# Kernel optimization log

Measured on AMD Instinct MI355X. Metric: run time of the kernel, lower is better.

Reference implementation:

```python
import jax, jax.numpy as jnp
import numpy as np

TOP_K = 2


def setup_inputs() -> dict:
    key = jax.random.key(0)
    k1, k2, k3, k4, k5 = jax.random.split(key, 5)
    H, F, E = 1024, 2048, 8
    B, S = 2, 1024
    return {
        "hidden_states": jax.random.normal(k1, (B, S, H), dtype=jnp.float32),
        "gate_w": jax.random.normal(k2, (E, H), dtype=jnp.float32) * (1.0 / np.sqrt(H)),
        "w1": jax.random.normal(k3, (E, F, H), dtype=jnp.float32) * (1.0 / np.sqrt(H)),
        "w2": jax.random.normal(k4, (E, H, F), dtype=jnp.float32) * (1.0 / np.sqrt(F)),
        "w3": jax.random.normal(k5, (E, F, H), dtype=jnp.float32) * (1.0 / np.sqrt(H)),
    }


def reference(hidden_states, gate_w, w1, w2, w3):
    B, S, H = hidden_states.shape
    E = gate_w.shape[0]
    x = hidden_states.reshape(-1, H)  # [T, H]

    # Router: softmax in float32, top-k, renormalize (exact Mixtral math)
    router_logits = x @ gate_w.T  # [T, E]
    probs = jax.nn.softmax(router_logits.astype(jnp.float32), axis=-1)
    routing_weights, selected = jax.lax.top_k(probs, TOP_K)  # [T, K]
    routing_weights = routing_weights / routing_weights.sum(axis=-1, keepdims=True)
    routing_weights = routing_weights.astype(x.dtype)

    # Per-token combine weight for each expert: [T, E]
    combine = (jax.nn.one_hot(selected, E, dtype=x.dtype) * routing_weights[..., None]).sum(axis=1)

    # Dense grouped expert SwiGLU MLP (zero combine weight for unselected experts
    # makes this strictly equivalent to the gathered/dispatched computation)
    h = jnp.einsum('th,efh->etf', x, w1)   # [E, T, F]
    g = jnp.einsum('th,efh->etf', x, w3)   # [E, T, F]
    mid = jax.nn.silu(h) * g               # SwiGLU
    expert_out = jnp.einsum('etf,ehf->eth', mid, w2)  # [E, T, H]
    out = jnp.einsum('eth,te->th', expert_out, combine)  # weighted combine

    return out.reshape(B, S, H), router_logits
```

## Files before the change

kernel.cpp:

```cpp
#include <hip/hip_runtime.h>
#include <hip/hip_bf16.h>
#include <math.h>

#define H 1024
#define FF 2048
#define E 8
#define T 2048
#define NSLOT (2*T)
#define SLOT_PAD 128

#define WCONV_BLKS 12288
#define XCONV_BLKS 512
#define ROUTER_BLKS T
#define K1_BLKS (WCONV_BLKS + XCONV_BLKS + ROUTER_BLKS)

typedef __attribute__((ext_vector_type(8))) short s16x8;
typedef __attribute__((ext_vector_type(4))) float f32x4;
typedef __attribute__((ext_vector_type(4))) unsigned int u32x4;

static __device__ __forceinline__ unsigned short f2bf(float f) {
    union { float f; unsigned u; } v; v.f = f;
    unsigned r = v.u + 0x7fff + ((v.u >> 16) & 1);
    return (unsigned short)(r >> 16);
}
static __device__ __forceinline__ float bf2f(unsigned short s) {
    union { unsigned u; float f; } v; v.u = ((unsigned)s) << 16;
    return v.f;
}
static __device__ __forceinline__ unsigned pack2(float a, float b) {
    return (unsigned)f2bf(a) | ((unsigned)f2bf(b) << 16);
}

typedef __attribute__((address_space(3))) unsigned int lds_uint;
typedef const __attribute__((address_space(1))) unsigned int glob_uint;
static __device__ __forceinline__ void gl_lds16(const void* g, void* l) {
    __builtin_amdgcn_global_load_lds((glob_uint*)g, (lds_uint*)l, 16, 0, 0);
}

static __device__ __forceinline__ void expert_range(const int* __restrict__ counts,
                                                    int e, int& off, int& cnt) {
    int acc = 0;
    #pragma unroll
    for (int i = 0; i < E; ++i) {
        int c = counts[i];
        if (i < e) acc += c;
        if (i == e) cnt = c;
    }
    off = acc;
}

__global__ __launch_bounds__(256) void prep_kernel(
    const float* __restrict__ x, const float* __restrict__ gw,
    const float* __restrict__ w1, const float* __restrict__ w3,
    const float* __restrict__ w2,
    unsigned short* __restrict__ w1b, unsigned short* __restrict__ w3b,
    unsigned short* __restrict__ w2b, unsigned short* __restrict__ xb,
    float* __restrict__ logits_out, int* __restrict__ top_id,
    float* __restrict__ top_w, int* __restrict__ counts)
{
    int b = blockIdx.x;
    int tid = threadIdx.x;
    if (b < WCONV_BLKS + XCONV_BLKS) {
        const float* s; unsigned short* d; size_t i;
        if (b < WCONV_BLKS) {
            int r = b >> 12;
            s = (r == 0) ? w1 : (r == 1) ? w3 : w2;
            d = (r == 0) ? w1b : (r == 1) ? w3b : w2b;
            i = ((size_t)(b & 4095) * 256 + tid) * 16;
        } else {
            s = x; d = xb;
            i = ((size_t)(b - WCONV_BLKS) * 256 + tid) * 16;
        }
        f32x4 a0 = __builtin_nontemporal_load((const f32x4*)(s + i));
        f32x4 a1 = __builtin_nontemporal_load((const f32x4*)(s + i + 4));
        f32x4 a2 = __builtin_nontemporal_load((const f32x4*)(s + i + 8));
        f32x4 a3 = __builtin_nontemporal_load((const f32x4*)(s + i + 12));
        u32x4 r0, r1;
        r0.x = pack2(a0.x, a0.y); r0.y = pack2(a0.z, a0.w);
        r0.z = pack2(a1.x, a1.y); r0.w = pack2(a1.z, a1.w);
        r1.x = pack2(a2.x, a2.y); r1.y = pack2(a2.z, a2.w);
        r1.z = pack2(a3.x, a3.y); r1.w = pack2(a3.z, a3.w);
        *(u32x4*)(d + i) = r0;
        *(u32x4*)(d + i + 8) = r1;
        return;
    }
    int t = b - (WCONV_BLKS + XCONV_BLKS);
    int e = tid >> 5;
    int l32 = tid & 31;
    const float* xr = x + (size_t)t * H;
    const float* gr = gw + (size_t)e * H;
    float s = 0.f;
    for (int h = l32; h < H; h += 32) s += xr[h] * gr[h];
    for (int off = 16; off; off >>= 1) s += __shfl_down(s, off, 32);
    __shared__ float lg[E];
    if (l32 == 0) lg[e] = s;
    __syncthreads();
    if (tid < E) logits_out[(size_t)t * E + tid] = lg[tid];
    if (tid == 0) {
        int i1 = 0; float b1 = lg[0];
        for (int i = 1; i < E; ++i) if (lg[i] > b1) { b1 = lg[i]; i1 = i; }
        int i2 = -1; float b2 = -INFINITY;
        for (int i = 0; i < E; ++i) if (i != i1 && lg[i] > b2) { b2 = lg[i]; i2 = i; }
        float p2 = expf(b2 - b1);
        float inv = 1.f / (1.f + p2);
        top_id[2*t]   = i1;  top_id[2*t+1] = i2;
        top_w[2*t]    = inv; top_w[2*t+1]  = p2 * inv;
        atomicAdd(&counts[i1], 1);
        atomicAdd(&counts[i2], 1);
    }
}

__global__ __launch_bounds__(256) void assign_kernel(
    const int* __restrict__ top_id, const int* __restrict__ counts,
    int* __restrict__ cursors, int* __restrict__ top_pos,
    int* __restrict__ slot_token)
{
    int t = blockIdx.x * 256 + threadIdx.x;
    if (t >= T) return;
    int offs[E];
    {
        int acc = 0;
        #pragma unroll
        for (int i = 0; i < E; ++i) { offs[i] = acc; acc += counts[i]; }
    }
    #pragma unroll
    for (int k = 0; k < 2; ++k) {
        int e = top_id[2*t + k];
        int p = offs[e] + atomicAdd(&cursors[e], 1);
        top_pos[2*t + k] = p;
        slot_token[p] = t;
    }
}

__global__ __launch_bounds__(256) void gemm1_kernel(
    const unsigned short* __restrict__ xb, const int* __restrict__ slot_token,
    const unsigned short* __restrict__ w1b, const unsigned short* __restrict__ w3b,
    const int* __restrict__ counts, unsigned short* __restrict__ mid)
{
    int e = blockIdx.z;
    int off, cnt;
    expert_range(counts, e, off, cnt);
    int m0 = blockIdx.y * 128;
    if (m0 >= cnt) return;
    int f0 = blockIdx.x * 64;

    __shared__ __align__(16) unsigned short sx[128 * 64];
    __shared__ __align__(16) unsigned short s1[64 * 64];
    __shared__ __align__(16) unsigned short s3[64 * 64];

    int tid = threadIdx.x;
    int wv = tid >> 6, ln = tid & 63;
    int quad = ln >> 4, l16 = ln & 15;
    int wm = wv & 1, wn = wv >> 1;
    int xor7 = l16 & 7;

    const unsigned short* xsrc[4]; unsigned short* xdst[4];
    #pragma unroll
    for (int j = 0; j < 4; ++j) {
        int row = wv * 32 + j * 8 + (ln >> 3);
        int slot = off + m0 + row;
        if (m0 + row >= cnt) slot = off;
        int tok = slot_token[slot];
        int cl = (ln & 7) ^ (row & 7);
        xsrc[j] = xb + (size_t)tok * H + cl * 8;
        xdst[j] = &sx[(wv * 32 + j * 8) * 64];
    }
    const unsigned short *w1s[2], *w3s[2]; unsigned short *d1[2], *d3[2];
    #pragma unroll
    for (int j = 0; j < 2; ++j) {
        int row = wv * 16 + j * 8 + (ln >> 3);
        int cl = (ln & 7) ^ (row & 7);
        w1s[j] = w1b + ((size_t)e * FF + f0 + row) * H + cl * 8;
        w3s[j] = w3b + ((size_t)e * FF + f0 + row) * H + cl * 8;
        d1[j] = &s1[(wv * 16 + j * 8) * 64];
        d3[j] = &s3[(wv * 16 + j * 8) * 64];
    }

    f32x4 acc1[4][2], acc3[4][2];
    #pragma unroll
    for (int i = 0; i < 4; ++i)
        #pragma unroll
        for (int j = 0; j < 2; ++j) {
            acc1[i][j] = (f32x4){0.f, 0.f, 0.f, 0.f};
            acc3[i][j] = (f32x4){0.f, 0.f, 0.f, 0.f};
        }

    for (int k0 = 0; k0 < H; k0 += 64) {
        #pragma unroll
        for (int j = 0; j < 4; ++j) gl_lds16(xsrc[j] + k0, xdst[j]);
        #pragma unroll
        for (int j = 0; j < 2; ++j) { gl_lds16(w1s[j] + k0, d1[j]); gl_lds16(w3s[j] + k0, d3[j]); }
        __syncthreads();
        #pragma unroll
        for (int ks = 0; ks < 2; ++ks) {
            int cph = ((quad + 4 * ks) ^ xor7) << 3;
            s16x8 a[4], b1v[2], b3v[2];
            #pragma unroll
            for (int i = 0; i < 4; ++i)
                a[i] = *(const s16x8*)&sx[(wm * 64 + i * 16 + l16) * 64 + cph];
            #pragma unroll
            for (int j = 0; j < 2; ++j) {
                b1v[j] = *(const s16x8*)&s1[(wn * 32 + j * 16 + l16) * 64 + cph];
                b3v[j] = *(const s16x8*)&s3[(wn * 32 + j * 16 + l16) * 64 + cph];
            }
            #pragma unroll
            for (int i = 0; i < 4; ++i)
                #pragma unroll
                for (int j = 0; j < 2; ++j) {
                    acc1[i][j] = __builtin_amdgcn_mfma_f32_16x16x32_bf16(a[i], b1v[j], acc1[i][j], 0, 0, 0);
                    acc3[i][j] = __builtin_amdgcn_mfma_f32_16x16x32_bf16(a[i], b3v[j], acc3[i][j], 0, 0, 0);
                }
        }
        __syncthreads();
    }

    #pragma unroll
    for (int i = 0; i < 4; ++i) {
        #pragma unroll
        for (int r = 0; r < 4; ++r) {
            int row = wm * 64 + i * 16 + quad * 4 + r;
            if (m0 + row < cnt) {
                size_t base = (size_t)(off + m0 + row) * FF + f0 + wn * 32;
                #pragma unroll
                for (int j = 0; j < 2; ++j) {
                    float h = acc1[i][j][r];
                    float g = acc3[i][j][r];
                    float v = h / (1.f + __expf(-h)) * g;
                    mid[base + j * 16 + l16] = f2bf(v);
                }
            }
        }
    }
}

__global__ __launch_bounds__(256) void gemm2_kernel(
    const unsigned short* __restrict__ mid, const unsigned short* __restrict__ w2b,
    const int* __restrict__ counts, unsigned short* __restrict__ y)
{
    int e = blockIdx.z;
    int off, cnt;
    expert_range(counts, e, off, cnt);
    int m0 = blockIdx.y * 128;
    if (m0 >= cnt) return;
    int n0 = blockIdx.x * 64;

    __shared__ __align__(16) unsigned short sa[128 * 64];
    __shared__ __align__(16) unsigned short sb[64 * 64];

    int tid = threadIdx.x;
    int wv = tid >> 6, ln = tid & 63;
    int quad = ln >> 4, l16 = ln & 15;
    int wm = wv & 1, wn = wv >> 1;
    int xor7 = l16 & 7;

    const unsigned short* asrc[4]; unsigned short* adst[4];
    #pragma unroll
    for (int j = 0; j < 4; ++j) {
        int row = wv * 32 + j * 8 + (ln >> 3);
        int cl = (ln & 7) ^ (row & 7);
        asrc[j] = mid + (size_t)(off + m0 + row) * FF + cl * 8;
        adst[j] = &sa[(wv * 32 + j * 8) * 64];
    }
    const unsigned short* bsrc[2]; unsigned short* bdst[2];
    #pragma unroll
    for (int j = 0; j < 2; ++j) {
        int row = wv * 16 + j * 8 + (ln >> 3);
        int cl = (ln & 7) ^ (row & 7);
        bsrc[j] = w2b + ((size_t)e * H + n0 + row) * FF + cl * 8;
        bdst[j] = &sb[(wv * 16 + j * 8) * 64];
    }

    f32x4 acc[4][2];
    #pragma unroll
    for (int i = 0; i < 4; ++i)
        #pragma unroll
        for (int j = 0; j < 2; ++j) acc[i][j] = (f32x4){0.f, 0.f, 0.f, 0.f};

    for (int k0 = 0; k0 < FF; k0 += 64) {
        #pragma unroll
        for (int j = 0; j < 4; ++j) gl_lds16(asrc[j] + k0, adst[j]);
        #pragma unroll
        for (int j = 0; j < 2; ++j) gl_lds16(bsrc[j] + k0, bdst[j]);
        __syncthreads();
        #pragma unroll
        for (int ks = 0; ks < 2; ++ks) {
            int cph = ((quad + 4 * ks) ^ xor7) << 3;
            s16x8 a[4], b[2];
            #pragma unroll
            for (int i = 0; i < 4; ++i)
                a[i] = *(const s16x8*)&sa[(wm * 64 + i * 16 + l16) * 64 + cph];
            #pragma unroll
            for (int j = 0; j < 2; ++j)
                b[j] = *(const s16x8*)&sb[(wn * 32 + j * 16 + l16) * 64 + cph];
            #pragma unroll
            for (int i = 0; i < 4; ++i)
                #pragma unroll
                for (int j = 0; j < 2; ++j)
                    acc[i][j] = __builtin_amdgcn_mfma_f32_16x16x32_bf16(a[i], b[j], acc[i][j], 0, 0, 0);
        }
        __syncthreads();
    }

    #pragma unroll
    for (int i = 0; i < 4; ++i) {
        #pragma unroll
        for (int r = 0; r < 4; ++r) {
            int row = wm * 64 + i * 16 + quad * 4 + r;
            if (m0 + row < cnt) {
                size_t base = (size_t)(off + m0 + row) * H + n0 + wn * 32;
                #pragma unroll
                for (int j = 0; j < 2; ++j)
                    y[base + j * 16 + l16] = f2bf(acc[i][j][r]);
            }
        }
    }
}

__global__ __launch_bounds__(256) void combine_kernel(
    const unsigned short* __restrict__ y, const int* __restrict__ top_pos,
    const float* __restrict__ top_w, float* __restrict__ out)
{
    int t = blockIdx.x, tid = threadIdx.x;
    int p0 = top_pos[2*t], p1 = top_pos[2*t+1];
    float w0 = top_w[2*t], w1 = top_w[2*t+1];
    ushort4 a = ((const ushort4*)(y + (size_t)p0 * H))[tid];
    ushort4 b = ((const ushort4*)(y + (size_t)p1 * H))[tid];
    float4 o;
    o.x = w0 * bf2f(a.x) + w1 * bf2f(b.x);
    o.y = w0 * bf2f(a.y) + w1 * bf2f(b.y);
    o.z = w0 * bf2f(a.z) + w1 * bf2f(b.z);
    o.w = w0 * bf2f(a.w) + w1 * bf2f(b.w);
    ((float4*)(out + (size_t)t * H))[tid] = o;
}

extern "C" void kernel_launch(void* const* d_in, const int* in_sizes, int n_in,
                              void* d_out, int out_size, void* d_ws, size_t ws_size,
                              hipStream_t stream) {
    const float* x  = (const float*)d_in[0];
    const float* gw = (const float*)d_in[1];
    const float* w1 = (const float*)d_in[2];
    const float* w2 = (const float*)d_in[3];
    const float* w3 = (const float*)d_in[4];
    float* out    = (float*)d_out;
    float* logits = out + (size_t)T * H;

    int* counts      = (int*)d_ws;
    int* cursors     = counts + 8;
    int* top_id      = counts + 16;
    int* top_pos     = top_id + 2*T;
    int* slot_token  = top_pos + 2*T;
    float* top_w     = (float*)(slot_token + NSLOT);
    unsigned short* xb  = (unsigned short*)(top_w + 2*T);
    unsigned short* mid = xb  + (size_t)T * H;
    unsigned short* y   = mid + (size_t)(NSLOT + SLOT_PAD) * FF;
    unsigned short* w1b = y   + (size_t)NSLOT * H;
    unsigned short* w3b = w1b + (size_t)E * FF * H;
    unsigned short* w2b = w3b + (size_t)E * FF * H;

    (void)hipMemsetAsync(counts, 0, 16 * sizeof(int), stream);

    prep_kernel<<<K1_BLKS, 256, 0, stream>>>(x, gw, w1, w3, w2,
                                             w1b, w3b, w2b, xb,
                                             logits, top_id, top_w, counts);
    assign_kernel<<<(T + 255) / 256, 256, 0, stream>>>(top_id, counts, cursors,
                                                       top_pos, slot_token);
    gemm1_kernel<<<dim3(FF / 64, 16, E), 256, 0, stream>>>(xb, slot_token,
                                                           w1b, w3b, counts, mid);
    gemm2_kernel<<<dim3(H / 64, 16, E), 256, 0, stream>>>(mid, w2b, counts, y);
    combine_kernel<<<T, 256, 0, stream>>>(y, top_pos, top_w, out);
}
```

Baseline: 422.2 us.

## Widen expert GEMM N-tiles to 128 and use grid-stride weight conversion

Both grouped GEMM kernels now compute 128x128 output tiles instead of 128x64, so each wave keeps a 4x4 accumulator set and the A tile staged in LDS is reused across twice as many columns. This halves the number of blocks and the redundant loads of token/mid rows. The fp32-to-bf16 prep now uses a fixed 2048-block grid-stride loop over all weight and activation chunks, with plain loads instead of nontemporal ones. Register pressure in gemm1 roughly doubles (32 accumulator vectors), which may lower occupancy, and the smaller grid may underfill the GPU.

Measured after the change: 445.1 us. +5.4%, slower.

```diff
diff --git a/kernel.cpp b/kernel.cpp
--- a/kernel.cpp
+++ b/kernel.cpp
@@ -9,10 +9,11 @@
 #define NSLOT (2*T)
 #define SLOT_PAD 128
 
-#define WCONV_BLKS 12288
-#define XCONV_BLKS 512
-#define ROUTER_BLKS T
-#define K1_BLKS (WCONV_BLKS + XCONV_BLKS + ROUTER_BLKS)
+#define WELEM (E*FF*H)
+#define XELEM (T*H)
+#define TOT_CHUNKS ((3*(size_t)WELEM + XELEM) / 8)
+#define CONV_BLKS 2048
+#define K1_BLKS (CONV_BLKS + T)
 
 typedef __attribute__((ext_vector_type(8))) short s16x8;
 typedef __attribute__((ext_vector_type(4))) float f32x4;
@@ -29,6 +30,12 @@
 }
 static __device__ __forceinline__ unsigned pack2(float a, float b) {
     return (unsigned)f2bf(a) | ((unsigned)f2bf(b) << 16);
+}
+static __device__ __forceinline__ u32x4 pack8(f32x4 a, f32x4 b) {
+    u32x4 r;
+    r.x = pack2(a.x, a.y); r.y = pack2(a.z, a.w);
+    r.z = pack2(b.x, b.y); r.w = pack2(b.z, b.w);
+    return r;
 }
 
 typedef __attribute__((address_space(3))) unsigned int lds_uint;
@@ -60,31 +67,22 @@
 {
     int b = blockIdx.x;
     int tid = threadIdx.x;
-    if (b < WCONV_BLKS + XCONV_BLKS) {
-        const float* s; unsigned short* d; size_t i;
-        if (b < WCONV_BLKS) {
-            int r = b >> 12;
-            s = (r == 0) ? w1 : (r == 1) ? w3 : w2;
-            d = (r == 0) ? w1b : (r == 1) ? w3b : w2b;
-            i = ((size_t)(b & 4095) * 256 + tid) * 16;
-        } else {
-            s = x; d = xb;
-            i = ((size_t)(b - WCONV_BLKS) * 256 + tid) * 16;
-        }
-        f32x4 a0 = __builtin_nontemporal_load((const f32x4*)(s + i));
-        f32x4 a1 = __builtin_nontemporal_load((const f32x4*)(s + i + 4));
-        f32x4 a2 = __builtin_nontemporal_load((const f32x4*)(s + i + 8));
-        f32x4 a3 = __builtin_nontemporal_load((const f32x4*)(s + i + 12));
-        u32x4 r0, r1;
-        r0.x = pack2(a0.x, a0.y); r0.y = pack2(a0.z, a0.w);
-        r0.z = pack2(a1.x, a1.y); r0.w = pack2(a1.z, a1.w);
-        r1.x = pack2(a2.x, a2.y); r1.y = pack2(a2.z, a2.w);
-        r1.z = pack2(a3.x, a3.y); r1.w = pack2(a3.z, a3.w);
-        *(u32x4*)(d + i) = r0;
-        *(u32x4*)(d + i + 8) = r1;
+    if (b < CONV_BLKS) {
+        for (size_t c = (size_t)b * 256 + tid; c < TOT_CHUNKS; c += (size_t)CONV_BLKS * 256) {
+            size_t base = c * 8;
+            int tsel = (int)(base >> 24);
+            const float* s; unsigned short* d; size_t o;
+            if (tsel == 0)      { s = w1; d = w1b; o = base; }
+            else if (tsel == 1) { s = w3; d = w3b; o = base - (size_t)WELEM; }
+            else if (tsel == 2) { s = w2; d = w2b; o = base - 2*(size_t)WELEM; }
+            else                { s = x;  d = xb;  o = base - 3*(size_t)WELEM; }
+            f32x4 a0 = *(const f32x4*)(s + o);
+            f32x4 a1 = *(const f32x4*)(s + o + 4);
+            *(u32x4*)(d + o) = pack8(a0, a1);
+        }
         return;
     }
-    int t = b - (WCONV_BLKS + XCONV_BLKS);
+    int t = b - CONV_BLKS;
     int e = tid >> 5;
     int l32 = tid & 31;
     const float* xr = x + (size_t)t * H;
@@ -142,11 +140,11 @@
     expert_range(counts, e, off, cnt);
     int m0 = blockIdx.y * 128;
     if (m0 >= cnt) return;
-    int f0 = blockIdx.x * 64;
+    int f0 = blockIdx.x * 128;
 
     __shared__ __align__(16) unsigned short sx[128 * 64];
-    __shared__ __align__(16) unsigned short s1[64 * 64];
-    __shared__ __align__(16) unsigned short s3[64 * 64];
+    __shared__ __align__(16) unsigned short s1[128 * 64];
+    __shared__ __align__(16) unsigned short s3[128 * 64];
 
     int tid = threadIdx.x;
     int wv = tid >> 6, ln = tid & 63;
@@ -165,48 +163,50 @@
         xsrc[j] = xb + (size_t)tok * H + cl * 8;
         xdst[j] = &sx[(wv * 32 + j * 8) * 64];
     }
-    const unsigned short *w1s[2], *w3s[2]; unsigned short *d1[2], *d3[2];
-    #pragma unroll
-    for (int j = 0; j < 2; ++j) {
-        int row = wv * 16 + j * 8 + (ln >> 3);
+    const unsigned short *w1s[4], *w3s[4]; unsigned short *d1[4], *d3[4];
+    #pragma unroll
+    for (int j = 0; j < 4; ++j) {
+        int row = wv * 32 + j * 8 + (ln >> 3);
         int cl = (ln & 7) ^ (row & 7);
         w1s[j] = w1b + ((size_t)e * FF + f0 + row) * H + cl * 8;
         w3s[j] = w3b + ((size_t)e * FF + f0 + row) * H + cl * 8;
-        d1[j] = &s1[(wv * 16 + j * 8) * 64];
-        d3[j] = &s3[(wv * 16 + j * 8) * 64];
-    }
-
-    f32x4 acc1[4][2], acc3[4][2];
+        d1[j] = &s1[(wv * 32 + j * 8) * 64];
+        d3[j] = &s3[(wv * 32 + j * 8) * 64];
+    }
+
+    f32x4 acc1[4][4], acc3[4][4];
     #pragma unroll
     for (int i = 0; i < 4; ++i)
         #pragma unroll
-        for (int j = 0; j < 2; ++j) {
+        for (int j = 0; j < 4; ++j) {
             acc1[i][j] = (f32x4){0.f, 0.f, 0.f, 0.f};
             acc3[i][j] = (f32x4){0.f, 0.f, 0.f, 0.f};
         }
 
     for (int k0 = 0; k0 < H; k0 += 64) {
         #pragma unroll
-        for (int j = 0; j < 4; ++j) gl_lds16(xsrc[j] + k0, xdst[j]);
-        #pragma unroll
-        for (int j = 0; j < 2; ++j) { gl_lds16(w1s[j] + k0, d1[j]); gl_lds16(w3s[j] + k0, d3[j]); }
+        for (int j = 0; j < 4; ++j) {
+            gl_lds16(xsrc[j] + k0, xdst[j]);
+            gl_lds16(w1s[j] + k0, d1[j]);
+            gl_lds16(w3s[j] + k0, d3[j]);
+        }
         __syncthreads();
         #pragma unroll
         for (int ks = 0; ks < 2; ++ks) {
             int cph = ((quad + 4 * ks) ^ xor7) << 3;
-            s16x8 a[4], b1v[2], b3v[2];
+            s16x8 a[4], b1v[4], b3v[4];
             #pragma unroll
             for (int i = 0; i < 4; ++i)
                 a[i] = *(const s16x8*)&sx[(wm * 64 + i * 16 + l16) * 64 + cph];
             #pragma unroll
-            for (int j = 0; j < 2; ++j) {
-                b1v[j] = *(const s16x8*)&s1[(wn * 32 + j * 16 + l16) * 64 + cph];
-                b3v[j] = *(const s16x8*)&s3[(wn * 32 + j * 16 + l16) * 64 + cph];
+            for (int j = 0; j < 4; ++j) {
+                b1v[j] = *(const s16x8*)&s1[(wn * 64 + j * 16 + l16) * 64 + cph];
+                b3v[j] = *(const s16x8*)&s3[(wn * 64 + j * 16 + l16) * 64 + cph];
             }
             #pragma unroll
             for (int i = 0; i < 4; ++i)
                 #pragma unroll
-                for (int j = 0; j < 2; ++j) {
+                for (int j = 0; j < 4; ++j) {
                     acc1[i][j] = __builtin_amdgcn_mfma_f32_16x16x32_bf16(a[i], b1v[j], acc1[i][j], 0, 0, 0);
                     acc3[i][j] = __builtin_amdgcn_mfma_f32_16x16x32_bf16(a[i], b3v[j], acc3[i][j], 0, 0, 0);
                 }
@@ -220,9 +220,9 @@
         for (int r = 0; r < 4; ++r) {
             int row = wm * 64 + i * 16 + quad * 4 + r;
             if (m0 + row < cnt) {
-                size_t base = (size_t)(off + m0 + row) * FF + f0 + wn * 32;
+                size_t base = (size_t)(off + m0 + row) * FF + f0 + wn * 64;
                 #pragma unroll
-                for (int j = 0; j < 2; ++j) {
+                for (int j = 0; j < 4; ++j) {
                     float h = acc1[i][j][r];
                     float g = acc3[i][j][r];
                     float v = h / (1.f + __expf(-h)) * g;
@@ -242,10 +242,10 @@
     expert_range(counts, e, off, cnt);
     int m0 = blockIdx.y * 128;
     if (m0 >= cnt) return;
-    int n0 = blockIdx.x * 64;
+    int n0 = blockIdx.x * 128;
 
     __shared__ __align__(16) unsigned short sa[128 * 64];
-    __shared__ __align__(16) unsigned short sb[64 * 64];
+    __shared__ __align__(16) unsigned short sb[128 * 64];
 
     int tid = threadIdx.x;
     int wv = tid >> 6, ln = tid & 63;
@@ -261,41 +261,42 @@
         asrc[j] = mid + (size_t)(off + m0 + row) * FF + cl * 8;
         adst[j] = &sa[(wv * 32 + j * 8) * 64];
     }
-    const unsigned short* bsrc[2]; unsigned short* bdst[2];
-    #pragma unroll
-    for (int j = 0; j < 2; ++j) {
-        int row = wv * 16 + j * 8 + (ln >> 3);
+    const unsigned short* bsrc[4]; unsigned short* bdst[4];
+    #pragma unroll
+    for (int j = 0; j < 4; ++j) {
+        int row = wv * 32 + j * 8 + (ln >> 3);
         int cl = (ln & 7) ^ (row & 7);
         bsrc[j] = w2b + ((size_t)e * H + n0 + row) * FF + cl * 8;
-        bdst[j] = &sb[(wv * 16 + j * 8) * 64];
-    }
-
-    f32x4 acc[4][2];
+        bdst[j] = &sb[(wv * 32 + j * 8) * 64];
+    }
+
+    f32x4 acc[4][4];
     #pragma unroll
     for (int i = 0; i < 4; ++i)
         #pragma unroll
-        for (int j = 0; j < 2; ++j) acc[i][j] = (f32x4){0.f, 0.f, 0.f, 0.f};
+        for (int j = 0; j < 4; ++j) acc[i][j] = (f32x4){0.f, 0.f, 0.f, 0.f};
 
     for (int k0 = 0; k0 < FF; k0 += 64) {
         #pragma unroll
-        for (int j = 0; j < 4; ++j) gl_lds16(asrc[j] + k0, adst[j]);
-        #pragma unroll
-        for (int j = 0; j < 2; ++j) gl_lds16(bsrc[j] + k0, bdst[j]);
+        for (int j = 0; j < 4; ++j) {
+            gl_lds16(asrc[j] + k0, adst[j]);
+            gl_lds16(bsrc[j] + k0, bdst[j]);
+        }
         __syncthreads();
         #pragma unroll
         for (int ks = 0; ks < 2; ++ks) {
             int cph = ((quad + 4 * ks) ^ xor7) << 3;
-            s16x8 a[4], b[2];
+            s16x8 a[4], b[4];
             #pragma unroll
             for (int i = 0; i < 4; ++i)
                 a[i] = *(const s16x8*)&sa[(wm * 64 + i * 16 + l16) * 64 + cph];
             #pragma unroll
-            for (int j = 0; j < 2; ++j)
-                b[j] = *(const s16x8*)&sb[(wn * 32 + j * 16 + l16) * 64 + cph];
+            for (int j = 0; j < 4; ++j)
+                b[j] = *(const s16x8*)&sb[(wn * 64 + j * 16 + l16) * 64 + cph];
             #pragma unroll
             for (int i = 0; i < 4; ++i)
                 #pragma unroll
-                for (int j = 0; j < 2; ++j)
+                for (int j = 0; j < 4; ++j)
                     acc[i][j] = __builtin_amdgcn_mfma_f32_16x16x32_bf16(a[i], b[j], acc[i][j], 0, 0, 0);
         }
         __syncthreads();
@@ -307,9 +308,9 @@
         for (int r = 0; r < 4; ++r) {
             int row = wm * 64 + i * 16 + quad * 4 + r;
             if (m0 + row < cnt) {
-                size_t base = (size_t)(off + m0 + row) * H + n0 + wn * 32;
+                size_t base = (size_t)(off + m0 + row) * H + n0 + wn * 64;
                 #pragma unroll
-                for (int j = 0; j < 2; ++j)
+                for (int j = 0; j < 4; ++j)
                     y[base + j * 16 + l16] = f2bf(acc[i][j][r]);
             }
         }
@@ -354,8 +355,8 @@
     unsigned short* mid = xb  + (size_t)T * H;
     unsigned short* y   = mid + (size_t)(NSLOT + SLOT_PAD) * FF;
     unsigned short* w1b = y   + (size_t)NSLOT * H;
-    unsigned short* w3b = w1b + (size_t)E * FF * H;
-    unsigned short* w2b = w3b + (size_t)E * FF * H;
+    unsigned short* w3b = w1b + (size_t)WELEM;
+    unsigned short* w2b = w3b + (size_t)WELEM;
 
     (void)hipMemsetAsync(counts, 0, 16 * sizeof(int), stream);
 
@@ -364,8 +365,8 @@
                                              logits, top_id, top_w, counts);
     assign_kernel<<<(T + 255) / 256, 256, 0, stream>>>(top_id, counts, cursors,
                                                        top_pos, slot_token);
-    gemm1_kernel<<<dim3(FF / 64, 16, E), 256, 0, stream>>>(xb, slot_token,
-                                                           w1b, w3b, counts, mid);
-    gemm2_kernel<<<dim3(H / 64, 16, E), 256, 0, stream>>>(mid, w2b, counts, y);
+    gemm1_kernel<<<dim3(FF / 128, 16, E), 256, 0, stream>>>(xb, slot_token,
+                                                            w1b, w3b, counts, mid);
+    gemm2_kernel<<<dim3(H / 128, 16, E), 256, 0, stream>>>(mid, w2b, counts, y);
     combine_kernel<<<T, 256, 0, stream>>>(y, top_pos, top_w, out);
 }
```
